# Optimization experiments

Hardware: AMD Instinct MI355X
Metric: run time of the kernel (lower is better)

The kernel has to match this reference:

```python
import jax, jax.numpy as jnp
import numpy as np
from jax import lax

NUM_BLOCKS = 3
NUM_LAYERS = 10
NL = NUM_BLOCKS * NUM_LAYERS  # 30 res blocks
RC = 512   # residual channels
GC = 512   # gate channels
SC = 512   # skip channels
KS = 2     # kernel size
CIN = 128  # local-conditioning channels
FRONT = 32 # front conv kernel size
OUT = 2    # gaussian (mean, log_std)
UPS = [16, 16]  # upsample scales, product = 256 hop
SQRT_HALF = 0.7071067811865476


def causal_conv1d(x, w, b, dilation):
    # x: [B,C_in,T], w: [C_out,C_in,K] -> left-pad only == torch pad-both + trim right (causal SAME)
    pad = dilation * (w.shape[-1] - 1)
    y = lax.conv_general_dilated(x, w, window_strides=(1,), padding=[(pad, 0)],
                                 rhs_dilation=(dilation,),
                                 dimension_numbers=('NCH', 'OIH', 'NCH'))
    return y + b[None, :, None]


def pw(x, w, b):
    # 1x1 conv: w [C_out,C_in]
    return jnp.einsum('oi,bit->bot', w, x) + b[None, :, None]


def upsample(c, up_w, up_b):
    # c: [B,CIN,Tm]; torch ConvTranspose2d(1,1,(3,2s),pad=(1,s//2),stride=(1,s)) + LeakyReLU(0.4)
    h = c[:, None]  # [B,1,CIN,Tm]
    for j, s in enumerate(UPS):
        k = up_w[j][:, :, ::-1, ::-1]  # flip kernel: transposed conv as lhs-dilated conv
        pw_ = 2 * s - 1 - s // 2       # = K - 1 - torch_pad along width
        h = lax.conv_general_dilated(h, k, window_strides=(1, 1),
                                     padding=[(1, 1), (pw_, pw_)],
                                     lhs_dilation=(1, s),
                                     dimension_numbers=('NCHW', 'OIHW', 'NCHW')) + up_b[j]
        h = jnp.where(h > 0, h, 0.4 * h)  # LeakyReLU(0.4)
    return h[:, 0]  # [B,CIN,T]


def setup_inputs() -> dict:
    key = jax.random.key(0)
    ks = iter(jax.random.split(key, 32))
    def rn(shape, scale):
        return jax.random.normal(next(ks), shape, dtype=jnp.float32) * scale
    B, T_mel = 1, 16
    T = T_mel * 256
    return {
        'x': rn((B, 1, T), 1.0),
        'c': rn((B, CIN, T_mel), 1.0),
        'front_w': rn((RC, 1, FRONT), 0.2),
        'front_b': rn((RC,), 0.05),
        'filt_w': rn((NL, GC, RC, KS), 0.03),
        'filt_b': rn((NL, GC), 0.05),
        'gate_w': rn((NL, GC, RC, KS), 0.03),
        'gate_b': rn((NL, GC), 0.05),
        'cf_w': rn((NL, GC, CIN), 0.05),
        'cf_b': rn((NL, GC), 0.05),
        'cg_w': rn((NL, GC, CIN), 0.05),
        'cg_b': rn((NL, GC), 0.05),
        'res_w': rn((NL, RC, GC), 0.04),
        'res_b': rn((NL, RC), 0.05),
        'skip_w': rn((NL, SC, GC), 0.04),
        'skip_b': rn((NL, SC), 0.05),
        'fin1_w': rn((SC, SC), 0.04),
        'fin1_b': rn((SC,), 0.05),
        'fin2_w': rn((OUT, SC), 0.04),
        'fin2_b': rn((OUT,), 0.05),
        'up_w': rn((2, 1, 1, 3, 2 * 16), 0.1),
        'up_b': rn((2,), 0.05),
    }


def reference(x, c, front_w, front_b, filt_w, filt_b, gate_w, gate_b,
              cf_w, cf_b, cg_w, cg_b, res_w, res_b, skip_w, skip_b,
              fin1_w, fin1_b, fin2_w, fin2_b, up_w, up_b):
    c_up = upsample(c, up_w, up_b)                       # [B,CIN,T]
    h = jax.nn.relu(causal_conv1d(x, front_w, front_b, 1))  # [B,RC,T]
    skip = jnp.zeros((x.shape[0], SC, x.shape[2]), x.dtype)
    for i in range(NL):
        d = KS ** (i % NUM_LAYERS)
        f = causal_conv1d(h, filt_w[i], filt_b[i], d) + pw(c_up, cf_w[i], cf_b[i])
        g = causal_conv1d(h, gate_w[i], gate_b[i], d) + pw(c_up, cg_w[i], cg_b[i])
        o = jnp.tanh(f) * jax.nn.sigmoid(g)
        h = (h + pw(o, res_w[i], res_b[i])) * SQRT_HALF
        skip = skip + pw(o, skip_w[i], skip_b[i])
    out = jax.nn.relu(skip)
    out = jax.nn.relu(pw(out, fin1_w, fin1_b))
    return pw(out, fin2_w, fin2_b)  # [B,OUT,T]
```

## Files before the change

kernel.cpp:

```cpp
#include <hip/hip_runtime.h>
#include <hip/hip_bf16.h>

#define TLEN 4096
#define HPADT 512
#define SQRT_HALF 0.70710678118654752f

typedef __attribute__((ext_vector_type(8))) short short8;
typedef __attribute__((ext_vector_type(4))) float floatx4;
typedef __attribute__((ext_vector_type(4))) unsigned short ushort4v;

#define MFMA_BF16(a, b, c) __builtin_amdgcn_mfma_f32_16x16x32_bf16((a), (b), (c), 0, 0, 0)

__device__ __forceinline__ float bf2f(unsigned short u) {
  union { unsigned int i; float f; } v; v.i = ((unsigned int)u) << 16; return v.f;
}
__device__ __forceinline__ unsigned short f2bf(float x) {
  union { float f; unsigned int i; } v; v.f = x;
  unsigned int r = v.i + 0x7FFFu + ((v.i >> 16) & 1u);
  return (unsigned short)(r >> 16);
}
__device__ __forceinline__ short8 ld8(const unsigned short* p) { return *(const short8*)p; }

template <int NI>
__device__ __forceinline__ void stage128(unsigned short* lds, const unsigned short* src,
                                         int stride, int tid) {
  #pragma unroll
  for (int inst = 0; inst < NI; ++inst) {
    int qb = inst * 256 + (tid & 192);
    int q = qb + (tid & 63);
    int r = q >> 4;
    int c = (q & 15) ^ (r & 15);
    __builtin_amdgcn_global_load_lds(
        (const __attribute__((address_space(1))) unsigned int*)(src + (size_t)r * stride + (c << 3)),
        (__attribute__((address_space(3))) unsigned int*)(lds + qb * 8),
        16, 0, 0);
  }
}
__device__ __forceinline__ short8 frag128(const unsigned short* lds, int r, int cj) {
  return *(const short8*)(lds + r * 128 + ((cj ^ (r & 15)) << 3));
}

template <int NI>
__device__ __forceinline__ void stage64(unsigned short* lds, const unsigned short* src,
                                        int stride, int tid) {
  #pragma unroll
  for (int inst = 0; inst < NI; ++inst) {
    int qb = inst * 256 + (tid & 192);
    int q = qb + (tid & 63);
    int r = q >> 3;
    int c = (q & 7) ^ (r & 7);
    __builtin_amdgcn_global_load_lds(
        (const __attribute__((address_space(1))) unsigned int*)(src + (size_t)r * stride + (c << 3)),
        (__attribute__((address_space(3))) unsigned int*)(lds + qb * 8),
        16, 0, 0);
  }
}
__device__ __forceinline__ short8 frag64(const unsigned short* lds, int r, int cj) {
  return *(const short8*)(lds + r * 64 + ((cj ^ (r & 7)) << 3));
}

__global__ __launch_bounds__(256) void cast_all_kernel(
    const float* __restrict__ fw, const float* __restrict__ gw,
    const float* __restrict__ rw, const float* __restrict__ sw,
    const float* __restrict__ cf, const float* __restrict__ cg,
    const float* __restrict__ f1, const float* __restrict__ fb,
    const float* __restrict__ cfb, const float* __restrict__ gb,
    const float* __restrict__ cgb,
    unsigned short* __restrict__ WA, unsigned short* __restrict__ RS,
    unsigned short* __restrict__ CA, unsigned short* __restrict__ F1c,
    float* __restrict__ fgb)
{
  int b = blockIdx.x;
  if (b < 7680) {
    size_t idx = (size_t)b * 256 + threadIdx.x;
    size_t l = idx >> 16;
    int o = (int)((idx >> 7) & 511);
    int i4 = (int)(idx & 127) * 4;
    const float4* fp = (const float4*)(fw + (((l * 512 + o) * 512 + i4) * 2));
    const float4* gp = (const float4*)(gw + (((l * 512 + o) * 512 + i4) * 2));
    float4 f0 = fp[0], f1v = fp[1];
    float4 g0 = gp[0], g1 = gp[1];
    size_t base0 = ((l * 2 + 0) * 1024);
    size_t base1 = ((l * 2 + 1) * 1024);
    *(ushort4v*)&WA[(base0 + o) * 512 + i4]       = (ushort4v){f2bf(f0.x), f2bf(f0.z), f2bf(f1v.x), f2bf(f1v.z)};
    *(ushort4v*)&WA[(base1 + o) * 512 + i4]       = (ushort4v){f2bf(f0.y), f2bf(f0.w), f2bf(f1v.y), f2bf(f1v.w)};
    *(ushort4v*)&WA[(base0 + 512 + o) * 512 + i4] = (ushort4v){f2bf(g0.x), f2bf(g0.z), f2bf(g1.x), f2bf(g1.z)};
    *(ushort4v*)&WA[(base1 + 512 + o) * 512 + i4] = (ushort4v){f2bf(g0.y), f2bf(g0.w), f2bf(g1.y), f2bf(g1.w)};
  } else if (b < 15360) {
    size_t idx = (size_t)(b - 7680) * 256 + threadIdx.x;
    size_t l = idx >> 16;
    int o = (int)((idx >> 7) & 511);
    int i4 = (int)(idx & 127) * 4;
    float4 r4 = *(const float4*)(rw + ((l * 512 + o) * 512 + i4));
    float4 s4 = *(const float4*)(sw + ((l * 512 + o) * 512 + i4));
    *(ushort4v*)&RS[(l * 1024 + o) * 512 + i4]       = (ushort4v){f2bf(r4.x), f2bf(r4.y), f2bf(r4.z), f2bf(r4.w)};
    *(ushort4v*)&RS[(l * 1024 + 512 + o) * 512 + i4] = (ushort4v){f2bf(s4.x), f2bf(s4.y), f2bf(s4.z), f2bf(s4.w)};
  } else if (b < 17280) {
    size_t idx = (size_t)(b - 15360) * 256 + threadIdx.x;
    size_t l = idx >> 14;
    int o = (int)((idx >> 5) & 511);
    int i4 = (int)(idx & 31) * 4;
    float4 f4 = *(const float4*)(cf + ((l * 512 + o) * 128 + i4));
    float4 g4 = *(const float4*)(cg + ((l * 512 + o) * 128 + i4));
    *(ushort4v*)&CA[(l * 1024 + o) * 128 + i4]       = (ushort4v){f2bf(f4.x), f2bf(f4.y), f2bf(f4.z), f2bf(f4.w)};
    *(ushort4v*)&CA[(l * 1024 + 512 + o) * 128 + i4] = (ushort4v){f2bf(g4.x), f2bf(g4.y), f2bf(g4.z), f2bf(g4.w)};
  } else if (b < 17536) {
    size_t idx = (size_t)(b - 17280) * 256 + threadIdx.x;
    float4 v = *(const float4*)(f1 + idx * 4);
    *(ushort4v*)&F1c[idx * 4] = (ushort4v){f2bf(v.x), f2bf(v.y), f2bf(v.z), f2bf(v.w)};
  } else {
    int idx = (b - 17536) * 256 + threadIdx.x;
    int l = idx >> 10, r = idx & 1023;
    float v;
    if (r < 512) v = fb[l * 512 + r] + cfb[l * 512 + r];
    else         v = gb[l * 512 + r - 512] + cgb[l * 512 + r - 512];
    fgb[idx] = v;
  }
}


__global__ __launch_bounds__(256) void upsample1_kernel(
    const float* __restrict__ c, const float* __restrict__ up_w,
    const float* __restrict__ up_b, float* __restrict__ u1)
{
  int x = threadIdx.x;
  int h = blockIdx.x;
  const float* w = up_w;
  float acc = 0.f;
  int k1 = (23 - x) & 15;
  #pragma unroll
  for (int dk = 0; dk < 2; ++dk) {
    int kx = k1 + 16 * dk;
    int num = x + kx - 23;
    if (num >= 0) {
      int qq = num >> 4;
      if (qq < 16) {
        #pragma unroll
        for (int ky = 0; ky < 3; ++ky) {
          int hh = h + ky - 1;
          if (hh >= 0 && hh < 128)
            acc += c[hh * 16 + qq] * w[(2 - ky) * 32 + (31 - kx)];
        }
      }
    }
  }
  acc += up_b[0];
  u1[h * 256 + x] = acc > 0.f ? acc : 0.4f * acc;
}

__global__ __launch_bounds__(256) void upsample2_kernel(
    const float* __restrict__ u1, const float* __restrict__ up_w,
    const float* __restrict__ up_b, unsigned short* __restrict__ cu)
{
  int x = blockIdx.x * 256 + threadIdx.x;
  int h = blockIdx.y;
  const float* w = up_w + 96;
  float acc = 0.f;
  int k1 = (23 - x) & 15;
  #pragma unroll
  for (int dk = 0; dk < 2; ++dk) {
    int kx = k1 + 16 * dk;
    int num = x + kx - 23;
    if (num >= 0) {
      int qq = num >> 4;
      if (qq < 256) {
        #pragma unroll
        for (int ky = 0; ky < 3; ++ky) {
          int hh = h + ky - 1;
          if (hh >= 0 && hh < 128)
            acc += u1[hh * 256 + qq] * w[(2 - ky) * 32 + (31 - kx)];
        }
      }
    }
  }
  acc += up_b[1];
  acc = acc > 0.f ? acc : 0.4f * acc;
  cu[(size_t)x * 128 + h] = f2bf(acc);
}

__global__ __launch_bounds__(256) void front_kernel(
    const float* __restrict__ x, const float* __restrict__ fw, const float* __restrict__ fb,
    float* __restrict__ hf, unsigned short* __restrict__ hbf)
{
  __shared__ float xs[40];
  int tid = threadIdx.x;
  int o = blockIdx.y * 256 + tid;
  int t0 = blockIdx.x * 8;
  if (tid < 39) {
    int gx = t0 - 31 + tid;
    xs[tid] = (gx >= 0) ? x[gx] : 0.f;
  }
  __syncthreads();
  float w[32];
  #pragma unroll
  for (int k = 0; k < 32; ++k) w[k] = fw[o * 32 + k];
  float b = fb[o];
  #pragma unroll
  for (int j = 0; j < 8; ++j) {
    float acc = b;
    #pragma unroll
    for (int k = 0; k < 32; ++k) acc += w[k] * xs[j + k];
    acc = acc > 0.f ? acc : 0.f;
    int t = t0 + j;
    hf[(size_t)t * 512 + o] = acc;
    hbf[(size_t)(HPADT + t) * 512 + o] = f2bf(acc);
  }
}

__global__ __launch_bounds__(256, 2) void gemm_a_kernel(
    const unsigned short* __restrict__ WA,
    const unsigned short* __restrict__ CA,
    const float* __restrict__ fgb,
    const unsigned short* __restrict__ hbf,
    const unsigned short* __restrict__ cu,
    unsigned short* __restrict__ obf,
    const int d)
{
  __shared__ unsigned short Af[2][32 * 64];
  __shared__ unsigned short Ag[2][32 * 64];
  __shared__ unsigned short Xs[2][128 * 64];

  const int tid = threadIdx.x;
  const int lane = tid & 63;
  const int wave = tid >> 6;
  const int lm = lane & 15, qd = lane >> 4;
  const int n0 = blockIdx.x * 128;
  const int m0 = blockIdx.y * 32;
  const int wn = wave * 32;

  floatx4 accF[2][2], accG[2][2];
  #pragma unroll
  for (int a = 0; a < 2; ++a)
    #pragma unroll
    for (int b = 0; b < 2; ++b) {
      accF[a][b] = (floatx4){0.f, 0.f, 0.f, 0.f};
      accG[a][b] = (floatx4){0.f, 0.f, 0.f, 0.f};
    }

  auto stage_step = [&](int s, int b) {
    if (s < 16) {
      int tap = s >> 3;
      int k0 = (s & 7) * 64;
      const unsigned short* ab = WA + (size_t)tap * 524288;
      stage64<1>(&Af[b][0], ab + (size_t)m0 * 512 + k0, 512, tid);
      stage64<1>(&Ag[b][0], ab + (size_t)(512 + m0) * 512 + k0, 512, tid);
      stage64<4>(&Xs[b][0], hbf + (size_t)(HPADT + n0 - (tap ? 0 : d)) * 512 + k0, 512, tid);
    } else {
      int k0 = (s - 16) * 64;
      stage64<1>(&Af[b][0], CA + (size_t)m0 * 128 + k0, 128, tid);
      stage64<1>(&Ag[b][0], CA + (size_t)(512 + m0) * 128 + k0, 128, tid);
      stage64<4>(&Xs[b][0], cu + (size_t)n0 * 128 + k0, 128, tid);
    }
  };

  stage_step(0, 0);
  for (int s = 0; s < 18; ++s) {
    __syncthreads();
    if (s < 17) stage_step(s + 1, (s + 1) & 1);
    const unsigned short* af = &Af[s & 1][0];
    const unsigned short* ag = &Ag[s & 1][0];
    const unsigned short* xs = &Xs[s & 1][0];
    #pragma unroll
    for (int j = 0; j < 2; ++j) {
      int cj = j * 4 + qd;
      short8 a0 = frag64(af, lm, cj);
      short8 a1 = frag64(af, 16 + lm, cj);
      short8 g0 = frag64(ag, lm, cj);
      short8 g1 = frag64(ag, 16 + lm, cj);
      short8 x0 = frag64(xs, wn + lm, cj);
      short8 x1 = frag64(xs, wn + 16 + lm, cj);
      accF[0][0] = MFMA_BF16(a0, x0, accF[0][0]);
      accF[0][1] = MFMA_BF16(a0, x1, accF[0][1]);
      accF[1][0] = MFMA_BF16(a1, x0, accF[1][0]);
      accF[1][1] = MFMA_BF16(a1, x1, accF[1][1]);
      accG[0][0] = MFMA_BF16(g0, x0, accG[0][0]);
      accG[0][1] = MFMA_BF16(g0, x1, accG[0][1]);
      accG[1][0] = MFMA_BF16(g1, x0, accG[1][0]);
      accG[1][1] = MFMA_BF16(g1, x1, accG[1][1]);
    }
  }

  #pragma unroll
  for (int mt = 0; mt < 2; ++mt) {
    int oc0 = m0 + mt * 16 + qd * 4;
    floatx4 fb4 = *(const floatx4*)&fgb[oc0];
    floatx4 gb4 = *(const floatx4*)&fgb[512 + oc0];
    #pragma unroll
    for (int nt = 0; nt < 2; ++nt) {
      int t = n0 + wn + nt * 16 + lm;
      ushort4v o4;
      #pragma unroll
      for (int r = 0; r < 4; ++r) {
        float f = accF[mt][nt][r] + fb4[r];
        float g = accG[mt][nt][r] + gb4[r];
        float ef = __expf(-2.f * f);
        float th = (1.f - ef) / (1.f + ef);
        float sg = 1.f / (1.f + __expf(-g));
        o4[r] = f2bf(th * sg);
      }
      *(ushort4v*)&obf[(size_t)t * 512 + oc0] = o4;
    }
  }
}

__global__ __launch_bounds__(256, 2) void gemm_b_kernel(
    const unsigned short* __restrict__ RS,
    const float* __restrict__ rb, const float* __restrict__ sb,
    const unsigned short* __restrict__ obf,
    float* __restrict__ hf, unsigned short* __restrict__ hbf,
    float* __restrict__ skip, unsigned short* __restrict__ skipbf,
    const int first, const int last)
{
  __shared__ unsigned short Ar[2][32 * 64];
  __shared__ unsigned short As_[2][32 * 64];
  __shared__ unsigned short Xs[2][128 * 64];

  const int tid = threadIdx.x;
  const int lane = tid & 63;
  const int wave = tid >> 6;
  const int lm = lane & 15, qd = lane >> 4;
  const int n0 = blockIdx.x * 128;
  const int m0 = blockIdx.y * 32;
  const int wn = wave * 32;

  floatx4 accR[2][2], accS[2][2];
  #pragma unroll
  for (int a = 0; a < 2; ++a)
    #pragma unroll
    for (int b = 0; b < 2; ++b) {
      accR[a][b] = (floatx4){0.f, 0.f, 0.f, 0.f};
      accS[a][b] = (floatx4){0.f, 0.f, 0.f, 0.f};
    }

  auto stage_step = [&](int s, int b) {
    int k0 = s * 64;
    stage64<1>(&Ar[b][0], RS + (size_t)m0 * 512 + k0, 512, tid);
    stage64<1>(&As_[b][0], RS + (size_t)(512 + m0) * 512 + k0, 512, tid);
    stage64<4>(&Xs[b][0], obf + (size_t)n0 * 512 + k0, 512, tid);
  };

  stage_step(0, 0);
  for (int s = 0; s < 8; ++s) {
    __syncthreads();
    if (s < 7) stage_step(s + 1, (s + 1) & 1);
    const unsigned short* ar = &Ar[s & 1][0];
    const unsigned short* as = &As_[s & 1][0];
    const unsigned short* xs = &Xs[s & 1][0];
    #pragma unroll
    for (int j = 0; j < 2; ++j) {
      int cj = j * 4 + qd;
      short8 a0 = frag64(ar, lm, cj);
      short8 a1 = frag64(ar, 16 + lm, cj);
      short8 g0 = frag64(as, lm, cj);
      short8 g1 = frag64(as, 16 + lm, cj);
      short8 x0 = frag64(xs, wn + lm, cj);
      short8 x1 = frag64(xs, wn + 16 + lm, cj);
      accR[0][0] = MFMA_BF16(a0, x0, accR[0][0]);
      accR[0][1] = MFMA_BF16(a0, x1, accR[0][1]);
      accR[1][0] = MFMA_BF16(a1, x0, accR[1][0]);
      accR[1][1] = MFMA_BF16(a1, x1, accR[1][1]);
      accS[0][0] = MFMA_BF16(g0, x0, accS[0][0]);
      accS[0][1] = MFMA_BF16(g0, x1, accS[0][1]);
      accS[1][0] = MFMA_BF16(g1, x0, accS[1][0]);
      accS[1][1] = MFMA_BF16(g1, x1, accS[1][1]);
    }
  }

  #pragma unroll
  for (int mt = 0; mt < 2; ++mt) {
    int oc0 = m0 + mt * 16 + qd * 4;
    floatx4 rb4 = *(const floatx4*)&rb[oc0];
    floatx4 sb4 = *(const floatx4*)&sb[oc0];
    #pragma unroll
    for (int nt = 0; nt < 2; ++nt) {
      int t = n0 + wn + nt * 16 + lm;
      size_t base = (size_t)t * 512 + oc0;
      floatx4 h4 = *(const floatx4*)&hf[base];
      floatx4 s4;
      if (first) s4 = (floatx4){0.f, 0.f, 0.f, 0.f};
      else s4 = *(const floatx4*)&skip[base];
      ushort4v hb4;
      #pragma unroll
      for (int r = 0; r < 4; ++r) {
        float hv = (h4[r] + accR[mt][nt][r] + rb4[r]) * SQRT_HALF;
        h4[r] = hv;
        hb4[r] = f2bf(hv);
        s4[r] = s4[r] + accS[mt][nt][r] + sb4[r];
      }
      *(floatx4*)&hf[base] = h4;
      *(ushort4v*)&hbf[(size_t)(HPADT + t) * 512 + oc0] = hb4;
      *(floatx4*)&skip[base] = s4;
      if (last) {
        ushort4v sk4;
        #pragma unroll
        for (int r = 0; r < 4; ++r) sk4[r] = f2bf(s4[r] > 0.f ? s4[r] : 0.f);
        *(ushort4v*)&skipbf[base] = sk4;
      }
    }
  }
}

__global__ __launch_bounds__(256) void final1_kernel(
    const unsigned short* __restrict__ W1,
    const float* __restrict__ b1,
    const unsigned short* __restrict__ skipbf,
    unsigned short* __restrict__ t1)
{
  __shared__ unsigned short Aw[2][64 * 128];
  __shared__ unsigned short Xs[2][128 * 128];

  const int tid = threadIdx.x;
  const int lane = tid & 63;
  const int wave = tid >> 6;
  const int lm = lane & 15, qd = lane >> 4;
  const int n0 = blockIdx.x * 128;
  const int m0 = blockIdx.y * 64;
  const int wm = (wave & 1) * 32;
  const int wn = (wave >> 1) * 64;

  floatx4 acc[2][4];
  #pragma unroll
  for (int a = 0; a < 2; ++a)
    #pragma unroll
    for (int b = 0; b < 4; ++b) acc[a][b] = (floatx4){0.f, 0.f, 0.f, 0.f};

  auto stage_step = [&](int s, int b) {
    int k0 = s * 128;
    stage128<4>(&Aw[b][0], W1 + (size_t)m0 * 512 + k0, 512, tid);
    stage128<8>(&Xs[b][0], skipbf + (size_t)n0 * 512 + k0, 512, tid);
  };

  stage_step(0, 0);
  for (int s = 0; s < 4; ++s) {
    __syncthreads();
    if (s < 3) stage_step(s + 1, (s + 1) & 1);
    const unsigned short* aw = &Aw[s & 1][0];
    const unsigned short* xs = &Xs[s & 1][0];
    #pragma unroll
    for (int j = 0; j < 4; ++j) {
      int cj = j * 4 + qd;
      short8 a[2], xv[4];
      a[0] = frag128(aw, wm + lm, cj);
      a[1] = frag128(aw, wm + 16 + lm, cj);
      #pragma unroll
      for (int nt = 0; nt < 4; ++nt) xv[nt] = frag128(xs, wn + nt * 16 + lm, cj);
      #pragma unroll
      for (int mt = 0; mt < 2; ++mt)
        #pragma unroll
        for (int nt = 0; nt < 4; ++nt)
          acc[mt][nt] = MFMA_BF16(a[mt], xv[nt], acc[mt][nt]);
    }
  }

  #pragma unroll
  for (int mt = 0; mt < 2; ++mt) {
    int oc0 = m0 + wm + mt * 16 + qd * 4;
    floatx4 b4 = *(const floatx4*)&b1[oc0];
    #pragma unroll
    for (int nt = 0; nt < 4; ++nt) {
      int t = n0 + wn + nt * 16 + lm;
      ushort4v o4;
      #pragma unroll
      for (int r = 0; r < 4; ++r) {
        float v = acc[mt][nt][r] + b4[r];
        o4[r] = f2bf(v > 0.f ? v : 0.f);
      }
      *(ushort4v*)&t1[(size_t)t * 512 + oc0] = o4;
    }
  }
}

__global__ __launch_bounds__(256) void final2_kernel(
    const float* __restrict__ W2, const float* __restrict__ b2,
    const unsigned short* __restrict__ t1, float* __restrict__ out)
{
  int wave = threadIdx.x >> 6, lane = threadIdx.x & 63;
  int t = blockIdx.x * 4 + wave;
  short8 v = ld8(t1 + (size_t)t * 512 + lane * 8);
  float a0 = 0.f, a1 = 0.f;
  #pragma unroll
  for (int r = 0; r < 8; ++r) {
    float f = bf2f((unsigned short)v[r]);
    a0 += W2[lane * 8 + r] * f;
    a1 += W2[512 + lane * 8 + r] * f;
  }
  #pragma unroll
  for (int off = 32; off > 0; off >>= 1) {
    a0 += __shfl_xor(a0, off, 64);
    a1 += __shfl_xor(a1, off, 64);
  }
  if (lane == 0) {
    out[t] = a0 + b2[0];
    out[TLEN + t] = a1 + b2[1];
  }
}

extern "C" void kernel_launch(void* const* d_in, const int* in_sizes, int n_in,
                              void* d_out, int out_size, void* d_ws, size_t ws_size,
                              hipStream_t stream) {
  (void)in_sizes; (void)n_in; (void)out_size; (void)ws_size;
  const float* x       = (const float*)d_in[0];
  const float* c       = (const float*)d_in[1];
  const float* front_w = (const float*)d_in[2];
  const float* front_b = (const float*)d_in[3];
  const float* filt_w  = (const float*)d_in[4];
  const float* filt_b  = (const float*)d_in[5];
  const float* gate_w  = (const float*)d_in[6];
  const float* gate_b  = (const float*)d_in[7];
  const float* cf_w    = (const float*)d_in[8];
  const float* cf_b    = (const float*)d_in[9];
  const float* cg_w    = (const float*)d_in[10];
  const float* cg_b    = (const float*)d_in[11];
  const float* res_w   = (const float*)d_in[12];
  const float* res_b   = (const float*)d_in[13];
  const float* skip_w  = (const float*)d_in[14];
  const float* skip_b  = (const float*)d_in[15];
  const float* fin1_w  = (const float*)d_in[16];
  const float* fin1_b  = (const float*)d_in[17];
  const float* fin2_w  = (const float*)d_in[18];
  const float* fin2_b  = (const float*)d_in[19];
  const float* up_w    = (const float*)d_in[20];
  const float* up_b    = (const float*)d_in[21];

  char* ws = (char*)d_ws;
  auto alloc = [&](size_t bytes) {
    char* p = ws;
    ws += (bytes + 255) & ~(size_t)255;
    return p;
  };
  unsigned short* WA     = (unsigned short*)alloc((size_t)30 * 2 * 1024 * 512 * 2);
  unsigned short* RS     = (unsigned short*)alloc((size_t)30 * 1024 * 512 * 2);
  unsigned short* CA     = (unsigned short*)alloc((size_t)30 * 1024 * 128 * 2);
  unsigned short* F1c    = (unsigned short*)alloc((size_t)512 * 512 * 2);
  float* fgb             = (float*)alloc((size_t)30 * 1024 * 4);
  float* u1              = (float*)alloc((size_t)128 * 256 * 4);
  unsigned short* cu     = (unsigned short*)alloc((size_t)TLEN * 128 * 2);
  float* hf              = (float*)alloc((size_t)TLEN * 512 * 4);
  unsigned short* hbf    = (unsigned short*)alloc((size_t)(HPADT + TLEN) * 512 * 2);
  unsigned short* obf    = (unsigned short*)alloc((size_t)TLEN * 512 * 2);
  float* skip            = (float*)alloc((size_t)TLEN * 512 * 4);
  unsigned short* skipbf = (unsigned short*)alloc((size_t)TLEN * 512 * 2);
  unsigned short* t1     = (unsigned short*)alloc((size_t)TLEN * 512 * 2);
  float* out             = (float*)d_out;

  hipMemsetAsync(hbf, 0, (size_t)HPADT * 512 * 2, stream);

  cast_all_kernel<<<17656, 256, 0, stream>>>(
      filt_w, gate_w, res_w, skip_w, cf_w, cg_w, fin1_w,
      filt_b, cf_b, gate_b, cg_b, WA, RS, CA, F1c, fgb);

  upsample1_kernel<<<dim3(128), 256, 0, stream>>>(c, up_w, up_b, u1);
  upsample2_kernel<<<dim3(16, 128), 256, 0, stream>>>(u1, up_w, up_b, cu);
  front_kernel<<<dim3(512, 2), 256, 0, stream>>>(x, front_w, front_b, hf, hbf);

  for (int l = 0; l < 30; ++l) {
    int d = 1 << (l % 10);
    gemm_a_kernel<<<dim3(32, 16), 256, 0, stream>>>(
        WA + (size_t)l * 2 * 524288, CA + (size_t)l * 131072,
        fgb + (size_t)l * 1024,
        hbf, cu, obf, d);
    gemm_b_kernel<<<dim3(32, 16), 256, 0, stream>>>(
        RS + (size_t)l * 524288,
        res_b + (size_t)l * 512, skip_b + (size_t)l * 512,
        obf, hf, hbf, skip, skipbf, (l == 0) ? 1 : 0, (l == 29) ? 1 : 0);
  }

  final1_kernel<<<dim3(32, 8), 256, 0, stream>>>(F1c, fin1_b, skipbf, t1);
  final2_kernel<<<1024, 256, 0, stream>>>(fin2_w, fin2_b, t1, out);
}
```

Before: 1.345 ms.

## Triple-buffer LDS staging with explicit vmcnt waits in both GEMM kernels

Moves both residual-block GEMM kernels from double to triple LDS buffering. Loads are issued two K-steps ahead, and partial s_waitcnt vmcnt counts replace the full-drain __syncthreads, so async global-to-LDS copies overlap more MFMA work. s_setprio is raised around the MFMA section. The cost is about 1.5x LDS per block, which could limit occupancy, plus a second barrier per step. Correctness depends on the hardcoded vmcnt values (6 loads per stage) matching the real instruction count.

```diff
diff --git a/kernel.cpp b/kernel.cpp
--- a/kernel.cpp
+++ b/kernel.cpp
@@ -58,6 +58,10 @@
 __device__ __forceinline__ short8 frag64(const unsigned short* lds, int r, int cj) {
   return *(const short8*)(lds + r * 64 + ((cj ^ (r & 7)) << 3));
 }
+
+__device__ __forceinline__ void wait_vm12() { asm volatile("s_waitcnt vmcnt(12)" ::: "memory"); }
+__device__ __forceinline__ void wait_vm6()  { asm volatile("s_waitcnt vmcnt(6)"  ::: "memory"); }
+__device__ __forceinline__ void wait_vm0()  { asm volatile("s_waitcnt vmcnt(0)"  ::: "memory"); }
 
 __global__ __launch_bounds__(256) void cast_all_kernel(
     const float* __restrict__ fw, const float* __restrict__ gw,
@@ -216,9 +220,9 @@
     unsigned short* __restrict__ obf,
     const int d)
 {
-  __shared__ unsigned short Af[2][32 * 64];
-  __shared__ unsigned short Ag[2][32 * 64];
-  __shared__ unsigned short Xs[2][128 * 64];
+  __shared__ unsigned short Af[3][32 * 64];
+  __shared__ unsigned short Ag[3][32 * 64];
+  __shared__ unsigned short Xs[3][128 * 64];
 
   const int tid = threadIdx.x;
   const int lane = tid & 63;
@@ -227,6 +231,7 @@
   const int n0 = blockIdx.x * 128;
   const int m0 = blockIdx.y * 32;
   const int wn = wave * 32;
+  const int NS = 18;
 
   floatx4 accF[2][2], accG[2][2];
   #pragma unroll
@@ -254,12 +259,21 @@
   };
 
   stage_step(0, 0);
-  for (int s = 0; s < 18; ++s) {
-    __syncthreads();
-    if (s < 17) stage_step(s + 1, (s + 1) & 1);
-    const unsigned short* af = &Af[s & 1][0];
-    const unsigned short* ag = &Ag[s & 1][0];
-    const unsigned short* xs = &Xs[s & 1][0];
+  stage_step(1, 1);
+  int cur = 0;
+  #pragma unroll 1
+  for (int s = 0; s < NS; ++s) {
+    int stg = cur + 2; if (stg >= 3) stg -= 3;
+    if (s + 2 < NS) stage_step(s + 2, stg);
+    if (s + 2 < NS)      wait_vm12();
+    else if (s + 1 < NS) wait_vm6();
+    else                 wait_vm0();
+    __builtin_amdgcn_s_barrier();
+    __builtin_amdgcn_sched_barrier(0);
+    const unsigned short* af = &Af[cur][0];
+    const unsigned short* ag = &Ag[cur][0];
+    const unsigned short* xs = &Xs[cur][0];
+    __builtin_amdgcn_s_setprio(1);
     #pragma unroll
     for (int j = 0; j < 2; ++j) {
       int cj = j * 4 + qd;
@@ -278,6 +292,11 @@
       accG[1][0] = MFMA_BF16(g1, x0, accG[1][0]);
       accG[1][1] = MFMA_BF16(g1, x1, accG[1][1]);
     }
+    __builtin_amdgcn_s_setprio(0);
+    __builtin_amdgcn_sched_barrier(0);
+    __builtin_amdgcn_s_barrier();
+    __builtin_amdgcn_sched_barrier(0);
+    cur = (cur == 2) ? 0 : cur + 1;
   }
 
   #pragma unroll
@@ -311,9 +330,9 @@
     float* __restrict__ skip, unsigned short* __restrict__ skipbf,
     const int first, const int last)
 {
-  __shared__ unsigned short Ar[2][32 * 64];
-  __shared__ unsigned short As_[2][32 * 64];
-  __shared__ unsigned short Xs[2][128 * 64];
+  __shared__ unsigned short Ar[3][32 * 64];
+  __shared__ unsigned short As_[3][32 * 64];
+  __shared__ unsigned short Xs[3][128 * 64];
 
   const int tid = threadIdx.x;
   const int lane = tid & 63;
@@ -322,6 +341,7 @@
   const int n0 = blockIdx.x * 128;
   const int m0 = blockIdx.y * 32;
   const int wn = wave * 32;
+  const int NS = 8;
 
   floatx4 accR[2][2], accS[2][2];
   #pragma unroll
@@ -340,12 +360,21 @@
   };
 
   stage_step(0, 0);
-  for (int s = 0; s < 8; ++s) {
-    __syncthreads();
-    if (s < 7) stage_step(s + 1, (s + 1) & 1);
-    const unsigned short* ar = &Ar[s & 1][0];
-    const unsigned short* as = &As_[s & 1][0];
-    const unsigned short* xs = &Xs[s & 1][0];
+  stage_step(1, 1);
+  int cur = 0;
+  #pragma unroll 1
+  for (int s = 0; s < NS; ++s) {
+    int stg = cur + 2; if (stg >= 3) stg -= 3;
+    if (s + 2 < NS) stage_step(s + 2, stg);
+    if (s + 2 < NS)      wait_vm12();
+    else if (s + 1 < NS) wait_vm6();
+    else                 wait_vm0();
+    __builtin_amdgcn_s_barrier();
+    __builtin_amdgcn_sched_barrier(0);
+    const unsigned short* ar = &Ar[cur][0];
+    const unsigned short* as = &As_[cur][0];
+    const unsigned short* xs = &Xs[cur][0];
+    __builtin_amdgcn_s_setprio(1);
     #pragma unroll
     for (int j = 0; j < 2; ++j) {
       int cj = j * 4 + qd;
@@ -364,6 +393,11 @@
       accS[1][0] = MFMA_BF16(g1, x0, accS[1][0]);
       accS[1][1] = MFMA_BF16(g1, x1, accS[1][1]);
     }
+    __builtin_amdgcn_s_setprio(0);
+    __builtin_amdgcn_sched_barrier(0);
+    __builtin_amdgcn_s_barrier();
+    __builtin_amdgcn_sched_barrier(0);
+    cur = (cur == 2) ? 0 : cur + 1;
   }
 
   #pragma unroll
```

Result: no change. 1.351 ms (+0.5%).
